# Kernel tuning notes

Measured on AMD Instinct MI355X. Metric: run time of the kernel, lower is better.

Reference implementation:

```python
import jax, jax.numpy as jnp
import numpy as np

# hyperparams (from init_kwargs / opt)
POS_W, NEG_W = 2.0, 40.0
MARGIN, THRESH = 0.1, 0.5
TAU, ALPHA, BETA = 4.0, 1.0, 0.5
N_EPOCHS = 100
F_STANDARD = False
N_CLASSES = 100


def setup_inputs() -> dict:
    key = jax.random.key(0)
    k1, k2, k3 = jax.random.split(key, 3)
    B, D = 4096, 128
    batch = jax.random.normal(k1, (B, D), dtype=jnp.float32)
    batch = batch / jnp.linalg.norm(batch, axis=1, keepdims=True)
    teacher = jax.random.normal(k2, (B, D), dtype=jnp.float32)
    teacher = teacher / jnp.linalg.norm(teacher, axis=1, keepdims=True)
    labels = jax.random.randint(k3, (B,), 0, N_CLASSES, dtype=jnp.int64 if jax.config.jax_enable_x64 else jnp.int32)
    return {"batch": batch, "teacher_batch": teacher, "labels": labels, "epoch": 50}


def reference(batch, teacher_batch, labels, epoch):
    B = batch.shape[0]
    sim = batch @ batch.T                              # [B,B]
    same = labels[:, None] == labels[None, :]          # [B,B]
    eye = jnp.eye(B, dtype=bool)
    pos = same & ~eye
    neg = ~same

    inf = jnp.float32(jnp.inf)
    min_pos = jnp.min(jnp.where(pos, sim, inf), axis=1)    # [B]
    max_neg = jnp.max(jnp.where(neg, sim, -inf), axis=1)   # [B]
    neg_keep = neg & (sim + MARGIN > min_pos[:, None])
    pos_keep = pos & (sim - MARGIN < max_neg[:, None])
    valid = jnp.any(neg_keep, axis=1) & jnp.any(pos_keep, axis=1)

    # masked log-sum-exp terms; exp(-inf)=0 keeps masked entries (and grads) zero
    pos_term = (1.0 / POS_W) * jnp.log1p(
        jnp.sum(jnp.exp(jnp.where(pos_keep, -POS_W * (sim - THRESH), -inf)), axis=1))
    neg_term = (1.0 / NEG_W) * jnp.log1p(
        jnp.sum(jnp.exp(jnp.where(neg_keep, NEG_W * (sim - THRESH), -inf)), axis=1))
    n_valid = jnp.maximum(jnp.sum(valid.astype(sim.dtype)), 1.0)
    loss_rank = jnp.sum(jnp.where(valid, pos_term + neg_term, 0.0)) / n_valid

    # KD term: per-anchor concat(pos_sims, neg_sims) is a permutation of the full
    # row, and softmax/KL are permutation invariant -> apply per-element scaling.
    t_sim = teacher_batch @ teacher_batch.T
    scale = jnp.ones_like(sim) if F_STANDARD else jnp.where(neg, BETA, 1.0)
    log_p = jax.nn.log_softmax(sim * scale / TAU, axis=1)
    q = jax.lax.stop_gradient(jax.nn.softmax(t_sim * scale / TAU, axis=1))
    # KLDivLoss(batchmean) on a [1,B] row == sum(q * (log q - log_p))
    kl_rows = jnp.sum(q * (jnp.log(q) - log_p), axis=1)   # [B]
    loss_kd = jnp.mean(kl_rows)

    loss = loss_rank + (epoch / N_EPOCHS) * ALPHA * (TAU ** 2) * loss_kd
    return (loss, loss_rank, loss_kd)
```

## Files before the change

kernel.cpp:

```cpp
#include <hip/hip_runtime.h>
#include <hip/hip_fp16.h>
#include <math.h>

#define BB  4096
#define DD  128
#define NCH 16
#define NP  8
#define TB  256

typedef __attribute__((ext_vector_type(8))) _Float16 half8;
typedef __attribute__((ext_vector_type(4))) float f32x4;

constexpr float POS_W  = 2.0f;
constexpr float NEG_W  = 40.0f;
constexpr float MARGIN = 0.1f;
constexpr float THRESH = 0.5f;

__device__ __forceinline__ unsigned short f2h(float f) {
  __half h = __float2half(f);
  return __half_as_ushort(h);
}
__device__ __forceinline__ f32x4 mfma16h(half8 a, half8 b, f32x4 c) {
  return __builtin_amdgcn_mfma_f32_16x16x32_f16(a, b, c, 0, 0, 0);
}
__device__ __forceinline__ void gll16(const void* g, void* l) {
  __builtin_amdgcn_global_load_lds(
      (const __attribute__((address_space(1))) void*)g,
      (__attribute__((address_space(3))) void*)l, 16, 0, 0);
}

__global__ __launch_bounds__(256) void k0(
    const float* __restrict__ b, const float* __restrict__ t,
    unsigned short* __restrict__ xf, unsigned short* __restrict__ yf)
{
  const int i = blockIdx.x * 256 + threadIdx.x;
  {
    float4 v = reinterpret_cast<const float4*>(b)[i];
    ushort4 h;
    h.x = f2h(v.x); h.y = f2h(v.y); h.z = f2h(v.z); h.w = f2h(v.w);
    reinterpret_cast<ushort4*>(xf)[i] = h;
  }
  {
    float4 v = reinterpret_cast<const float4*>(t)[i];
    ushort4 h;
    h.x = f2h(v.x); h.y = f2h(v.y); h.z = f2h(v.z); h.w = f2h(v.w);
    reinterpret_cast<ushort4*>(yf)[i] = h;
  }
}


__global__ __launch_bounds__(TB, 3) void kA(
    const unsigned short* __restrict__ xf,
    const int* __restrict__ labels,
    float* __restrict__ mpP, float* __restrict__ mnP, float* __restrict__ zsP)
{
  __shared__ unsigned short sX[2][4096];
  __shared__ int sJlab[256];

  const int tid  = threadIdx.x;
  const int lane = tid & 63;
  const int wid  = tid >> 6;
  const int ag   = blockIdx.x & 31;
  const int ch   = blockIdx.x >> 5;
  const int i0w  = ag * 128 + wid * 32;
  const int l15  = lane & 15;
  const int hi_l = lane >> 4;
  const int rbase = hi_l * 4;
  const int koff  = hi_l * 8;
  const int j0ch  = ch * 256;
  const int srow  = lane & 31;
  const int sk0   = wid * 32 + (lane >> 5) * 8;

  sJlab[tid] = labels[j0ch + tid];

  half8 Ax[2][4];
#pragma unroll
  for (int at = 0; at < 2; ++at) {
    const size_t ab = (size_t)(i0w + at * 16 + l15) * DD + koff;
#pragma unroll
    for (int s = 0; s < 4; ++s)
      Ax[at][s] = *reinterpret_cast<const half8*>(xf + ab + s * 32);
  }
  int labA[2][4];
#pragma unroll
  for (int at = 0; at < 2; ++at)
#pragma unroll
    for (int r = 0; r < 4; ++r) labA[at][r] = labels[i0w + at * 16 + rbase + r];

  float mp[2][4], mn[2][4], zs[2][4];
#pragma unroll
  for (int at = 0; at < 2; ++at)
#pragma unroll
    for (int r = 0; r < 4; ++r) { mp[at][r] = INFINITY; mn[at][r] = -INFINITY; zs[at][r] = 0.f; }

  {
    const size_t g0 = (size_t)(j0ch + srow) * DD + sk0;
    gll16(xf + g0,      &sX[0][wid * 1024]);
    gll16(xf + g0 + 16, &sX[0][wid * 1024 + 512]);
  }

#pragma unroll 1
  for (int pp = 0; pp < NP; ++pp) {
    const int cur = pp & 1;
    __syncthreads();
    if (pp + 1 < NP) {
      const size_t g0 = (size_t)(j0ch + (pp + 1) * 32 + srow) * DD + sk0;
      gll16(xf + g0,      &sX[cur ^ 1][wid * 1024]);
      gll16(xf + g0 + 16, &sX[cur ^ 1][wid * 1024 + 512]);
    }

    f32x4 acc[2][2];
#pragma unroll
    for (int at = 0; at < 2; ++at)
#pragma unroll
      for (int t = 0; t < 2; ++t) acc[at][t] = {0.f, 0.f, 0.f, 0.f};
#pragma unroll
    for (int s = 0; s < 4; ++s) {
#pragma unroll
      for (int t = 0; t < 2; ++t) {
        const int ro = (s * 128 + hi_l * 32 + t * 16 + l15) * 8;
        half8 vB = *reinterpret_cast<const half8*>(&sX[cur][ro]);
        acc[0][t] = mfma16h(Ax[0][s], vB, acc[0][t]);
        acc[1][t] = mfma16h(Ax[1][s], vB, acc[1][t]);
      }
    }

#pragma unroll
    for (int t = 0; t < 2; ++t) {
      const int lj   = sJlab[pp * 32 + t * 16 + l15];
      const int jcol = j0ch + pp * 32 + t * 16 + l15;
#pragma unroll
      for (int at = 0; at < 2; ++at)
#pragma unroll
        for (int r = 0; r < 4; ++r) {
          float sim = acc[at][t][r];
          bool same = (lj == labA[at][r]);
          zs[at][r] += __expf(sim * (same ? 0.25f : 0.125f));
          if (same) {
            if (jcol != i0w + at * 16 + rbase + r) mp[at][r] = fminf(mp[at][r], sim);
          } else {
            mn[at][r] = fmaxf(mn[at][r], sim);
          }
        }
    }
  }

#pragma unroll
  for (int at = 0; at < 2; ++at)
#pragma unroll
    for (int r = 0; r < 4; ++r)
#pragma unroll
      for (int m = 1; m < 16; m <<= 1) {
        mp[at][r] = fminf(mp[at][r], __shfl_xor(mp[at][r], m));
        mn[at][r] = fmaxf(mn[at][r], __shfl_xor(mn[at][r], m));
        zs[at][r] += __shfl_xor(zs[at][r], m);
      }
  if (l15 == 0) {
#pragma unroll
    for (int at = 0; at < 2; ++at)
#pragma unroll
      for (int r = 0; r < 4; ++r) {
        const int i_r = i0w + at * 16 + rbase + r;
        mpP[ch * BB + i_r] = mp[at][r];
        mnP[ch * BB + i_r] = mn[at][r];
        zsP[ch * BB + i_r] = zs[at][r];
      }
  }
}

__global__ __launch_bounds__(256) void kR(
    const float* __restrict__ mpP, const float* __restrict__ mnP,
    const float* __restrict__ zsP,
    float* __restrict__ mpg, float* __restrict__ mng, float* __restrict__ zsg,
    int* __restrict__ cnt)
{
  const int i = blockIdx.x * 256 + threadIdx.x;
  if (i == 0) *cnt = 0;
  float a = INFINITY, b = -INFINITY, c = 0.f;
#pragma unroll
  for (int ch = 0; ch < NCH; ++ch) {
    a = fminf(a, mpP[ch * BB + i]);
    b = fmaxf(b, mnP[ch * BB + i]);
    c += zsP[ch * BB + i];
  }
  mpg[i] = a; mng[i] = b; zsg[i] = c;
}

__global__ __launch_bounds__(TB, 2) void kB(
    const unsigned short* __restrict__ xf, const unsigned short* __restrict__ yf,
    const int* __restrict__ labels,
    const float* __restrict__ mpg, const float* __restrict__ mng,
    float* __restrict__ ztP, float* __restrict__ wvP,
    float* __restrict__ psP, float* __restrict__ nsP)
{
  __shared__ unsigned short sB[2][8192];
  __shared__ int sJlab[256];

  const int tid  = threadIdx.x;
  const int lane = tid & 63;
  const int wid  = tid >> 6;
  const int ag   = blockIdx.x & 31;
  const int ch   = blockIdx.x >> 5;
  const int i0w  = ag * 128 + wid * 32;
  const int l15  = lane & 15;
  const int hi_l = lane >> 4;
  const int rbase = hi_l * 4;
  const int koff  = hi_l * 8;
  const int j0ch  = ch * 256;
  const int srow  = lane & 31;
  const int sk0   = wid * 32 + (lane >> 5) * 8;

  sJlab[tid] = labels[j0ch + tid];

  half8 Ax[2][4], Ay[2][4];
#pragma unroll
  for (int at = 0; at < 2; ++at) {
    const size_t ab = (size_t)(i0w + at * 16 + l15) * DD + koff;
#pragma unroll
    for (int s = 0; s < 4; ++s) {
      Ax[at][s] = *reinterpret_cast<const half8*>(xf + ab + s * 32);
      Ay[at][s] = *reinterpret_cast<const half8*>(yf + ab + s * 32);
    }
  }
  int labA[2][4]; float mpA[2][4], mnA[2][4];
#pragma unroll
  for (int at = 0; at < 2; ++at)
#pragma unroll
    for (int r = 0; r < 4; ++r) {
      const int i_r = i0w + at * 16 + rbase + r;
      labA[at][r] = labels[i_r];
      mpA[at][r]  = mpg[i_r];
      mnA[at][r]  = mng[i_r];
    }

  float zt[2][4], wv[2][4], ps[2][4], ns[2][4];
#pragma unroll
  for (int at = 0; at < 2; ++at)
#pragma unroll
    for (int r = 0; r < 4; ++r) { zt[at][r] = 0.f; wv[at][r] = 0.f; ps[at][r] = 0.f; ns[at][r] = 0.f; }

  {
    const size_t g0 = (size_t)(j0ch + srow) * DD + sk0;
    gll16(xf + g0,      &sB[0][wid * 1024]);
    gll16(xf + g0 + 16, &sB[0][wid * 1024 + 512]);
    gll16(yf + g0,      &sB[0][4096 + wid * 1024]);
    gll16(yf + g0 + 16, &sB[0][4096 + wid * 1024 + 512]);
  }

#pragma unroll 1
  for (int pp = 0; pp < NP; ++pp) {
    const int cur = pp & 1;
    __syncthreads();
    if (pp + 1 < NP) {
      const size_t g0 = (size_t)(j0ch + (pp + 1) * 32 + srow) * DD + sk0;
      gll16(xf + g0,      &sB[cur ^ 1][wid * 1024]);
      gll16(xf + g0 + 16, &sB[cur ^ 1][wid * 1024 + 512]);
      gll16(yf + g0,      &sB[cur ^ 1][4096 + wid * 1024]);
      gll16(yf + g0 + 16, &sB[cur ^ 1][4096 + wid * 1024 + 512]);
    }

    f32x4 aS[2][2], aT[2][2];
#pragma unroll
    for (int at = 0; at < 2; ++at)
#pragma unroll
      for (int t = 0; t < 2; ++t) { aS[at][t] = {0.f,0.f,0.f,0.f}; aT[at][t] = {0.f,0.f,0.f,0.f}; }
#pragma unroll
    for (int s = 0; s < 4; ++s) {
#pragma unroll
      for (int t = 0; t < 2; ++t) {
        const int ro = (s * 128 + hi_l * 32 + t * 16 + l15) * 8;
        half8 vX = *reinterpret_cast<const half8*>(&sB[cur][ro]);
        half8 vY = *reinterpret_cast<const half8*>(&sB[cur][4096 + ro]);
        aS[0][t] = mfma16h(Ax[0][s], vX, aS[0][t]);
        aS[1][t] = mfma16h(Ax[1][s], vX, aS[1][t]);
        aT[0][t] = mfma16h(Ay[0][s], vY, aT[0][t]);
        aT[1][t] = mfma16h(Ay[1][s], vY, aT[1][t]);
      }
    }

#pragma unroll
    for (int t = 0; t < 2; ++t) {
      const int lj   = sJlab[pp * 32 + t * 16 + l15];
      const int jcol = j0ch + pp * 32 + t * 16 + l15;
#pragma unroll
      for (int at = 0; at < 2; ++at)
#pragma unroll
        for (int r = 0; r < 4; ++r) {
          float sim = aS[at][t][r], ts0 = aT[at][t][r];
          bool same = (lj == labA[at][r]);
          float sc = same ? 0.25f : 0.125f;
          float s  = sim * sc;
          float ts = ts0 * sc;
          float et = __expf(ts);
          zt[at][r] += et;
          wv[at][r] += et * (ts - s);
          if (same) {
            if (jcol != i0w + at * 16 + rbase + r && (sim - MARGIN < mnA[at][r]))
              ps[at][r] += __expf(-POS_W * (sim - THRESH));
          } else {
            if (sim + MARGIN > mpA[at][r])
              ns[at][r] += __expf(NEG_W * (sim - THRESH));
          }
        }
    }
  }

#pragma unroll
  for (int at = 0; at < 2; ++at)
#pragma unroll
    for (int r = 0; r < 4; ++r)
#pragma unroll
      for (int m = 1; m < 16; m <<= 1) {
        zt[at][r] += __shfl_xor(zt[at][r], m);
        wv[at][r] += __shfl_xor(wv[at][r], m);
        ps[at][r] += __shfl_xor(ps[at][r], m);
        ns[at][r] += __shfl_xor(ns[at][r], m);
      }
  if (l15 == 0) {
#pragma unroll
    for (int at = 0; at < 2; ++at)
#pragma unroll
      for (int r = 0; r < 4; ++r) {
        const int i_r = i0w + at * 16 + rbase + r;
        ztP[ch * BB + i_r] = zt[at][r];
        wvP[ch * BB + i_r] = wv[at][r];
        psP[ch * BB + i_r] = ps[at][r];
        nsP[ch * BB + i_r] = ns[at][r];
      }
  }
}

__global__ __launch_bounds__(512) void kD(
    const float* __restrict__ zsg, const float* __restrict__ ztP,
    const float* __restrict__ wvP, const float* __restrict__ psP,
    const float* __restrict__ nsP, const int* __restrict__ epoch,
    double* __restrict__ rkP, double* __restrict__ kdP, int* __restrict__ nvP,
    int* __restrict__ cnt, float* __restrict__ out)
{
  __shared__ double sR[8], sK[8];
  __shared__ int    sN[8];
  const int tid = threadIdx.x;
  const int lane = tid & 63;
  const int wid = tid >> 6;
  const int i = blockIdx.x * 512 + tid;

  float zt = 0.f, wv = 0.f, ps = 0.f, ns = 0.f;
#pragma unroll
  for (int c = 0; c < NCH; ++c) {
    zt += ztP[c * BB + i];
    wv += wvP[c * BB + i];
    ps += psP[c * BB + i];
    ns += nsP[c * BB + i];
  }
  float zs = zsg[i];
  double kd = (double)(wv / zt + __logf(zs) - __logf(zt));
  double rank = 0.0; int nv = 0;
  if (ps > 0.f && ns > 0.f) {
    rank = (double)(log1pf(ps) * 0.5f + log1pf(ns) * 0.025f);
    nv = 1;
  }
#pragma unroll
  for (int o = 32; o; o >>= 1) {
    rank += __shfl_xor(rank, o);
    kd   += __shfl_xor(kd, o);
    nv   += __shfl_xor(nv, o);
  }
  if (lane == 0) { sR[wid] = rank; sK[wid] = kd; sN[wid] = nv; }
  __syncthreads();
  if (tid == 0) {
    double R_ = 0.0, K_ = 0.0; int N_ = 0;
    for (int w = 0; w < 8; ++w) { R_ += sR[w]; K_ += sK[w]; N_ += sN[w]; }
    rkP[blockIdx.x] = R_;
    kdP[blockIdx.x] = K_;
    nvP[blockIdx.x] = N_;
    __threadfence();
    int old = atomicAdd(cnt, 1);
    if (old == 7) {
      __threadfence();
      double RT = 0.0, KT = 0.0; int NT = 0;
      for (int b = 0; b < 8; ++b) { RT += rkP[b]; KT += kdP[b]; NT += nvP[b]; }
      double loss_rank = RT / (double)(NT < 1 ? 1 : NT);
      double loss_kd   = KT / (double)BB;
      double wgt = (double)epoch[0] * 0.16;
      out[0] = (float)(loss_rank + wgt * loss_kd);
      out[1] = (float)loss_rank;
      out[2] = (float)loss_kd;
      *cnt = 0;
    }
  }
}

extern "C" void kernel_launch(void* const* d_in, const int* in_sizes, int n_in,
                              void* d_out, int out_size, void* d_ws, size_t ws_size,
                              hipStream_t stream)
{
  (void)in_sizes; (void)n_in; (void)out_size; (void)ws_size;
  const float* batch   = (const float*)d_in[0];
  const float* teacher = (const float*)d_in[1];
  const int*   labels  = (const int*)d_in[2];
  const int*   epoch   = (const int*)d_in[3];
  float* out = (float*)d_out;

  char* w = (char*)d_ws;
  const size_t MB = 1048576;
  unsigned short* xf = (unsigned short*)(w + 0 * MB);
  unsigned short* yf = (unsigned short*)(w + 1 * MB);
  const size_t PCH = (size_t)NCH * BB * sizeof(float);
  float* mpP = (float*)(w + 2 * MB + 0 * PCH);
  float* mnP = (float*)(w + 2 * MB + 1 * PCH);
  float* zsP = (float*)(w + 2 * MB + 2 * PCH);
  float* ztP = (float*)(w + 2 * MB + 3 * PCH);
  float* wvP = (float*)(w + 2 * MB + 4 * PCH);
  float* psP = (float*)(w + 2 * MB + 5 * PCH);
  float* nsP = (float*)(w + 2 * MB + 6 * PCH);
  float* mpg = (float*)(w + 4 * MB);
  float* mng = (float*)(w + 4 * MB + 16384);
  float* zsg = (float*)(w + 4 * MB + 32768);
  double* rkP = (double*)(w + 4 * MB + 49152);
  double* kdP = (double*)(w + 4 * MB + 49152 + 64);
  int*    nvP = (int*)(w + 4 * MB + 49152 + 128);
  int*    cnt = (int*)(w + 4 * MB + 49152 + 192);

  k0<<<dim3(BB * DD / 4 / 256), dim3(256), 0, stream>>>(batch, teacher, xf, yf);
  kA<<<dim3(32 * NCH), dim3(TB), 0, stream>>>(xf, labels, mpP, mnP, zsP);
  kR<<<dim3(BB / 256), dim3(256), 0, stream>>>(mpP, mnP, zsP, mpg, mng, zsg, cnt);
  kB<<<dim3(32 * NCH), dim3(TB), 0, stream>>>(xf, yf, labels, mpg, mng,
                                              ztP, wvP, psP, nsP);
  kD<<<dim3(8), dim3(512), 0, stream>>>(zsg, ztP, wvP, psP, nsP, epoch,
                                        rkP, kdP, nvP, cnt, out);
}
```

Before: 63.48 us.

## Move teacher GEMM into first pass and fold min/max reduction into second pass

The teacher similarity GEMM and its softmax partial sums move from the second similarity pass into the first, which now computes student and teacher tiles together. The separate reduction kernel kR is removed: the second pass reduces the per-chunk min-positive and max-negative partials itself into shared memory, and kD sums the zs partials directly. The counter reset moves into the conversion kernel. This saves one launch and rebalances work between the passes, but the first pass now carries more registers and LDS at lower occupancy, and every block of the second pass repeats the chunk reduction for its 128 anchors.

```diff
diff --git a/kernel.cpp b/kernel.cpp
--- a/kernel.cpp
+++ b/kernel.cpp
@@ -31,9 +31,11 @@
 
 __global__ __launch_bounds__(256) void k0(
     const float* __restrict__ b, const float* __restrict__ t,
-    unsigned short* __restrict__ xf, unsigned short* __restrict__ yf)
+    unsigned short* __restrict__ xf, unsigned short* __restrict__ yf,
+    int* __restrict__ cnt)
 {
   const int i = blockIdx.x * 256 + threadIdx.x;
+  if (i == 0) *cnt = 0;
   {
     float4 v = reinterpret_cast<const float4*>(b)[i];
     ushort4 h;
@@ -49,12 +51,13 @@
 }
 
 
-__global__ __launch_bounds__(TB, 3) void kA(
-    const unsigned short* __restrict__ xf,
+__global__ __launch_bounds__(TB, 2) void kG1(
+    const unsigned short* __restrict__ xf, const unsigned short* __restrict__ yf,
     const int* __restrict__ labels,
-    float* __restrict__ mpP, float* __restrict__ mnP, float* __restrict__ zsP)
+    float* __restrict__ zsP, float* __restrict__ mpP, float* __restrict__ mnP,
+    float* __restrict__ ztP, float* __restrict__ wvP)
 {
-  __shared__ unsigned short sX[2][4096];
+  __shared__ unsigned short sB[2][8192];
   __shared__ int sJlab[256];
 
   const int tid  = threadIdx.x;
@@ -73,13 +76,15 @@
 
   sJlab[tid] = labels[j0ch + tid];
 
-  half8 Ax[2][4];
+  half8 Ax[2][4], Ay[2][4];
 #pragma unroll
   for (int at = 0; at < 2; ++at) {
     const size_t ab = (size_t)(i0w + at * 16 + l15) * DD + koff;
 #pragma unroll
-    for (int s = 0; s < 4; ++s)
+    for (int s = 0; s < 4; ++s) {
       Ax[at][s] = *reinterpret_cast<const half8*>(xf + ab + s * 32);
+      Ay[at][s] = *reinterpret_cast<const half8*>(yf + ab + s * 32);
+    }
   }
   int labA[2][4];
 #pragma unroll
@@ -87,16 +92,21 @@
 #pragma unroll
     for (int r = 0; r < 4; ++r) labA[at][r] = labels[i0w + at * 16 + rbase + r];
 
-  float mp[2][4], mn[2][4], zs[2][4];
-#pragma unroll
-  for (int at = 0; at < 2; ++at)
-#pragma unroll
-    for (int r = 0; r < 4; ++r) { mp[at][r] = INFINITY; mn[at][r] = -INFINITY; zs[at][r] = 0.f; }
+  float zs[2][4], mp[2][4], mn[2][4], zt[2][4], wv[2][4];
+#pragma unroll
+  for (int at = 0; at < 2; ++at)
+#pragma unroll
+    for (int r = 0; r < 4; ++r) {
+      zs[at][r] = 0.f; mp[at][r] = INFINITY; mn[at][r] = -INFINITY;
+      zt[at][r] = 0.f; wv[at][r] = 0.f;
+    }
 
   {
     const size_t g0 = (size_t)(j0ch + srow) * DD + sk0;
-    gll16(xf + g0,      &sX[0][wid * 1024]);
-    gll16(xf + g0 + 16, &sX[0][wid * 1024 + 512]);
+    gll16(xf + g0,      &sB[0][wid * 1024]);
+    gll16(xf + g0 + 16, &sB[0][wid * 1024 + 512]);
+    gll16(yf + g0,      &sB[0][4096 + wid * 1024]);
+    gll16(yf + g0 + 16, &sB[0][4096 + wid * 1024 + 512]);
   }
 
 #pragma unroll 1
@@ -105,23 +115,28 @@
     __syncthreads();
     if (pp + 1 < NP) {
       const size_t g0 = (size_t)(j0ch + (pp + 1) * 32 + srow) * DD + sk0;
-      gll16(xf + g0,      &sX[cur ^ 1][wid * 1024]);
-      gll16(xf + g0 + 16, &sX[cur ^ 1][wid * 1024 + 512]);
-    }
-
-    f32x4 acc[2][2];
+      gll16(xf + g0,      &sB[cur ^ 1][wid * 1024]);
+      gll16(xf + g0 + 16, &sB[cur ^ 1][wid * 1024 + 512]);
+      gll16(yf + g0,      &sB[cur ^ 1][4096 + wid * 1024]);
+      gll16(yf + g0 + 16, &sB[cur ^ 1][4096 + wid * 1024 + 512]);
+    }
+
+    f32x4 aS[2][2], aT[2][2];
 #pragma unroll
     for (int at = 0; at < 2; ++at)
 #pragma unroll
-      for (int t = 0; t < 2; ++t) acc[at][t] = {0.f, 0.f, 0.f, 0.f};
+      for (int t = 0; t < 2; ++t) { aS[at][t] = {0.f,0.f,0.f,0.f}; aT[at][t] = {0.f,0.f,0.f,0.f}; }
 #pragma unroll
     for (int s = 0; s < 4; ++s) {
 #pragma unroll
       for (int t = 0; t < 2; ++t) {
         const int ro = (s * 128 + hi_l * 32 + t * 16 + l15) * 8;
-        half8 vB = *reinterpret_cast<const half8*>(&sX[cur][ro]);
-        acc[0][t] = mfma16h(Ax[0][s], vB, acc[0][t]);
-        acc[1][t] = mfma16h(Ax[1][s], vB, acc[1][t]);
+        half8 vX = *reinterpret_cast<const half8*>(&sB[cur][ro]);
+        half8 vY = *reinterpret_cast<const half8*>(&sB[cur][4096 + ro]);
+        aS[0][t] = mfma16h(Ax[0][s], vX, aS[0][t]);
+        aS[1][t] = mfma16h(Ax[1][s], vX, aS[1][t]);
+        aT[0][t] = mfma16h(Ay[0][s], vY, aT[0][t]);
+        aT[1][t] = mfma16h(Ay[1][s], vY, aT[1][t]);
       }
     }
 
@@ -133,9 +148,15 @@
       for (int at = 0; at < 2; ++at)
 #pragma unroll
         for (int r = 0; r < 4; ++r) {
-          float sim = acc[at][t][r];
+          float sim = aS[at][t][r], tsim = aT[at][t][r];
           bool same = (lj == labA[at][r]);
-          zs[at][r] += __expf(sim * (same ? 0.25f : 0.125f));
+          float sc = same ? 0.25f : 0.125f;
+          float s  = sim * sc;
+          float ts = tsim * sc;
+          zs[at][r] += __expf(s);
+          float et = __expf(ts);
+          zt[at][r] += et;
+          wv[at][r] += et * (ts - s);
           if (same) {
             if (jcol != i0w + at * 16 + rbase + r) mp[at][r] = fminf(mp[at][r], sim);
           } else {
@@ -151,9 +172,11 @@
     for (int r = 0; r < 4; ++r)
 #pragma unroll
       for (int m = 1; m < 16; m <<= 1) {
+        zs[at][r] += __shfl_xor(zs[at][r], m);
         mp[at][r] = fminf(mp[at][r], __shfl_xor(mp[at][r], m));
         mn[at][r] = fmaxf(mn[at][r], __shfl_xor(mn[at][r], m));
-        zs[at][r] += __shfl_xor(zs[at][r], m);
+        zt[at][r] += __shfl_xor(zt[at][r], m);
+        wv[at][r] += __shfl_xor(wv[at][r], m);
       }
   if (l15 == 0) {
 #pragma unroll
@@ -161,40 +184,24 @@
 #pragma unroll
       for (int r = 0; r < 4; ++r) {
         const int i_r = i0w + at * 16 + rbase + r;
+        zsP[ch * BB + i_r] = zs[at][r];
         mpP[ch * BB + i_r] = mp[at][r];
         mnP[ch * BB + i_r] = mn[at][r];
-        zsP[ch * BB + i_r] = zs[at][r];
-      }
-  }
-}
-
-__global__ __launch_bounds__(256) void kR(
+        ztP[ch * BB + i_r] = zt[at][r];
+        wvP[ch * BB + i_r] = wv[at][r];
+      }
+  }
+}
+
+__global__ __launch_bounds__(TB, 3) void kG2(
+    const unsigned short* __restrict__ xf,
+    const int* __restrict__ labels,
     const float* __restrict__ mpP, const float* __restrict__ mnP,
-    const float* __restrict__ zsP,
-    float* __restrict__ mpg, float* __restrict__ mng, float* __restrict__ zsg,
-    int* __restrict__ cnt)
-{
-  const int i = blockIdx.x * 256 + threadIdx.x;
-  if (i == 0) *cnt = 0;
-  float a = INFINITY, b = -INFINITY, c = 0.f;
-#pragma unroll
-  for (int ch = 0; ch < NCH; ++ch) {
-    a = fminf(a, mpP[ch * BB + i]);
-    b = fmaxf(b, mnP[ch * BB + i]);
-    c += zsP[ch * BB + i];
-  }
-  mpg[i] = a; mng[i] = b; zsg[i] = c;
-}
-
-__global__ __launch_bounds__(TB, 2) void kB(
-    const unsigned short* __restrict__ xf, const unsigned short* __restrict__ yf,
-    const int* __restrict__ labels,
-    const float* __restrict__ mpg, const float* __restrict__ mng,
-    float* __restrict__ ztP, float* __restrict__ wvP,
     float* __restrict__ psP, float* __restrict__ nsP)
 {
-  __shared__ unsigned short sB[2][8192];
+  __shared__ unsigned short sX[2][4096];
   __shared__ int sJlab[256];
+  __shared__ float sMPr[128], sMNr[128];
 
   const int tid  = threadIdx.x;
   const int lane = tid & 63;
@@ -210,42 +217,54 @@
   const int srow  = lane & 31;
   const int sk0   = wid * 32 + (lane >> 5) * 8;
 
+  {
+    const size_t g0 = (size_t)(j0ch + srow) * DD + sk0;
+    gll16(xf + g0,      &sX[0][wid * 1024]);
+    gll16(xf + g0 + 16, &sX[0][wid * 1024 + 512]);
+  }
+
   sJlab[tid] = labels[j0ch + tid];
-
-  half8 Ax[2][4], Ay[2][4];
+  if (tid < 128) {
+    const int aidx = ag * 128 + tid;
+    float a = INFINITY, b = -INFINITY;
+#pragma unroll
+    for (int c = 0; c < NCH; ++c) {
+      a = fminf(a, mpP[c * BB + aidx]);
+      b = fmaxf(b, mnP[c * BB + aidx]);
+    }
+    sMPr[tid] = a; sMNr[tid] = b;
+  }
+
+  half8 Ax[2][4];
 #pragma unroll
   for (int at = 0; at < 2; ++at) {
     const size_t ab = (size_t)(i0w + at * 16 + l15) * DD + koff;
 #pragma unroll
-    for (int s = 0; s < 4; ++s) {
+    for (int s = 0; s < 4; ++s)
       Ax[at][s] = *reinterpret_cast<const half8*>(xf + ab + s * 32);
-      Ay[at][s] = *reinterpret_cast<const half8*>(yf + ab + s * 32);
-    }
-  }
-  int labA[2][4]; float mpA[2][4], mnA[2][4];
+  }
+  int labA[2][4];
+#pragma unroll
+  for (int at = 0; at < 2; ++at)
+#pragma unroll
+    for (int r = 0; r < 4; ++r) labA[at][r] = labels[i0w + at * 16 + rbase + r];
+
+  __syncthreads();
+  float mpA[2][4], mnA[2][4];
 #pragma unroll
   for (int at = 0; at < 2; ++at)
 #pragma unroll
     for (int r = 0; r < 4; ++r) {
-      const int i_r = i0w + at * 16 + rbase + r;
-      labA[at][r] = labels[i_r];
-      mpA[at][r]  = mpg[i_r];
-      mnA[at][r]  = mng[i_r];
-    }
-
-  float zt[2][4], wv[2][4], ps[2][4], ns[2][4];
-#pragma unroll
-  for (int at = 0; at < 2; ++at)
-#pragma unroll
-    for (int r = 0; r < 4; ++r) { zt[at][r] = 0.f; wv[at][r] = 0.f; ps[at][r] = 0.f; ns[at][r] = 0.f; }
-
-  {
-    const size_t g0 = (size_t)(j0ch + srow) * DD + sk0;
-    gll16(xf + g0,      &sB[0][wid * 1024]);
-    gll16(xf + g0 + 16, &sB[0][wid * 1024 + 512]);
-    gll16(yf + g0,      &sB[0][4096 + wid * 1024]);
-    gll16(yf + g0 + 16, &sB[0][4096 + wid * 1024 + 512]);
-  }
+      const int al = wid * 32 + at * 16 + rbase + r;
+      mpA[at][r] = sMPr[al];
+      mnA[at][r] = sMNr[al];
+    }
+
+  float ps[2][4], ns[2][4];
+#pragma unroll
+  for (int at = 0; at < 2; ++at)
+#pragma unroll
+    for (int r = 0; r < 4; ++r) { ps[at][r] = 0.f; ns[at][r] = 0.f; }
 
 #pragma unroll 1
   for (int pp = 0; pp < NP; ++pp) {
@@ -253,28 +272,23 @@
     __syncthreads();
     if (pp + 1 < NP) {
       const size_t g0 = (size_t)(j0ch + (pp + 1) * 32 + srow) * DD + sk0;
-      gll16(xf + g0,      &sB[cur ^ 1][wid * 1024]);
-      gll16(xf + g0 + 16, &sB[cur ^ 1][wid * 1024 + 512]);
-      gll16(yf + g0,      &sB[cur ^ 1][4096 + wid * 1024]);
-      gll16(yf + g0 + 16, &sB[cur ^ 1][4096 + wid * 1024 + 512]);
-    }
-
-    f32x4 aS[2][2], aT[2][2];
+      gll16(xf + g0,      &sX[cur ^ 1][wid * 1024]);
+      gll16(xf + g0 + 16, &sX[cur ^ 1][wid * 1024 + 512]);
+    }
+
+    f32x4 acc[2][2];
 #pragma unroll
     for (int at = 0; at < 2; ++at)
 #pragma unroll
-      for (int t = 0; t < 2; ++t) { aS[at][t] = {0.f,0.f,0.f,0.f}; aT[at][t] = {0.f,0.f,0.f,0.f}; }
+      for (int t = 0; t < 2; ++t) acc[at][t] = {0.f, 0.f, 0.f, 0.f};
 #pragma unroll
     for (int s = 0; s < 4; ++s) {
 #pragma unroll
       for (int t = 0; t < 2; ++t) {
         const int ro = (s * 128 + hi_l * 32 + t * 16 + l15) * 8;
-        half8 vX = *reinterpret_cast<const half8*>(&sB[cur][ro]);
-        half8 vY = *reinterpret_cast<const half8*>(&sB[cur][4096 + ro]);
-        aS[0][t] = mfma16h(Ax[0][s], vX, aS[0][t]);
-        aS[1][t] = mfma16h(Ax[1][s], vX, aS[1][t]);
-        aT[0][t] = mfma16h(Ay[0][s], vY, aT[0][t]);
-        aT[1][t] = mfma16h(Ay[1][s], vY, aT[1][t]);
+        half8 vB = *reinterpret_cast<const half8*>(&sX[cur][ro]);
+        acc[0][t] = mfma16h(Ax[0][s], vB, acc[0][t]);
+        acc[1][t] = mfma16h(Ax[1][s], vB, acc[1][t]);
       }
     }
 
@@ -286,14 +300,8 @@
       for (int at = 0; at < 2; ++at)
 #pragma unroll
         for (int r = 0; r < 4; ++r) {
-          float sim = aS[at][t][r], ts0 = aT[at][t][r];
+          float sim = acc[at][t][r];
           bool same = (lj == labA[at][r]);
-          float sc = same ? 0.25f : 0.125f;
-          float s  = sim * sc;
-          float ts = ts0 * sc;
-          float et = __expf(ts);
-          zt[at][r] += et;
-          wv[at][r] += et * (ts - s);
           if (same) {
             if (jcol != i0w + at * 16 + rbase + r && (sim - MARGIN < mnA[at][r]))
               ps[at][r] += __expf(-POS_W * (sim - THRESH));
@@ -311,8 +319,6 @@
     for (int r = 0; r < 4; ++r)
 #pragma unroll
       for (int m = 1; m < 16; m <<= 1) {
-        zt[at][r] += __shfl_xor(zt[at][r], m);
-        wv[at][r] += __shfl_xor(wv[at][r], m);
         ps[at][r] += __shfl_xor(ps[at][r], m);
         ns[at][r] += __shfl_xor(ns[at][r], m);
       }
@@ -322,8 +328,6 @@
 #pragma unroll
       for (int r = 0; r < 4; ++r) {
         const int i_r = i0w + at * 16 + rbase + r;
-        ztP[ch * BB + i_r] = zt[at][r];
-        wvP[ch * BB + i_r] = wv[at][r];
         psP[ch * BB + i_r] = ps[at][r];
         nsP[ch * BB + i_r] = ns[at][r];
       }
@@ -331,7 +335,7 @@
 }
 
 __global__ __launch_bounds__(512) void kD(
-    const float* __restrict__ zsg, const float* __restrict__ ztP,
+    const float* __restrict__ zsP, const float* __restrict__ ztP,
     const float* __restrict__ wvP, const float* __restrict__ psP,
     const float* __restrict__ nsP, const int* __restrict__ epoch,
     double* __restrict__ rkP, double* __restrict__ kdP, int* __restrict__ nvP,
@@ -344,15 +348,15 @@
   const int wid = tid >> 6;
   const int i = blockIdx.x * 512 + tid;
 
-  float zt = 0.f, wv = 0.f, ps = 0.f, ns = 0.f;
+  float zs = 0.f, zt = 0.f, wv = 0.f, ps = 0.f, ns = 0.f;
 #pragma unroll
   for (int c = 0; c < NCH; ++c) {
+    zs += zsP[c * BB + i];
     zt += ztP[c * BB + i];
     wv += wvP[c * BB + i];
     ps += psP[c * BB + i];
     ns += nsP[c * BB + i];
   }
-  float zs = zsg[i];
   double kd = (double)(wv / zt + __logf(zs) - __logf(zt));
   double rank = 0.0; int nv = 0;
   if (ps > 0.f && ns > 0.f) {
@@ -406,26 +410,22 @@
   unsigned short* xf = (unsigned short*)(w + 0 * MB);
   unsigned short* yf = (unsigned short*)(w + 1 * MB);
   const size_t PCH = (size_t)NCH * BB * sizeof(float);
-  float* mpP = (float*)(w + 2 * MB + 0 * PCH);
-  float* mnP = (float*)(w + 2 * MB + 1 * PCH);
-  float* zsP = (float*)(w + 2 * MB + 2 * PCH);
+  float* zsP = (float*)(w + 2 * MB + 0 * PCH);
+  float* mpP = (float*)(w + 2 * MB + 1 * PCH);
+  float* mnP = (float*)(w + 2 * MB + 2 * PCH);
   float* ztP = (float*)(w + 2 * MB + 3 * PCH);
   float* wvP = (float*)(w + 2 * MB + 4 * PCH);
   float* psP = (float*)(w + 2 * MB + 5 * PCH);
   float* nsP = (float*)(w + 2 * MB + 6 * PCH);
-  float* mpg = (float*)(w + 4 * MB);
-  float* mng = (float*)(w + 4 * MB + 16384);
-  float* zsg = (float*)(w + 4 * MB + 32768);
-  double* rkP = (double*)(w + 4 * MB + 49152);
-  double* kdP = (double*)(w + 4 * MB + 49152 + 64);
-  int*    nvP = (int*)(w + 4 * MB + 49152 + 128);
-  int*    cnt = (int*)(w + 4 * MB + 49152 + 192);
-
-  k0<<<dim3(BB * DD / 4 / 256), dim3(256), 0, stream>>>(batch, teacher, xf, yf);
-  kA<<<dim3(32 * NCH), dim3(TB), 0, stream>>>(xf, labels, mpP, mnP, zsP);
-  kR<<<dim3(BB / 256), dim3(256), 0, stream>>>(mpP, mnP, zsP, mpg, mng, zsg, cnt);
-  kB<<<dim3(32 * NCH), dim3(TB), 0, stream>>>(xf, yf, labels, mpg, mng,
-                                              ztP, wvP, psP, nsP);
-  kD<<<dim3(8), dim3(512), 0, stream>>>(zsg, ztP, wvP, psP, nsP, epoch,
+  double* rkP = (double*)(w + 4 * MB);
+  double* kdP = (double*)(w + 4 * MB + 64);
+  int*    nvP = (int*)(w + 4 * MB + 128);
+  int*    cnt = (int*)(w + 4 * MB + 192);
+
+  k0<<<dim3(BB * DD / 4 / 256), dim3(256), 0, stream>>>(batch, teacher, xf, yf, cnt);
+  kG1<<<dim3(32 * NCH), dim3(TB), 0, stream>>>(xf, yf, labels,
+                                               zsP, mpP, mnP, ztP, wvP);
+  kG2<<<dim3(32 * NCH), dim3(TB), 0, stream>>>(xf, labels, mpP, mnP, psP, nsP);
+  kD<<<dim3(8), dim3(512), 0, stream>>>(zsP, ztP, wvP, psP, nsP, epoch,
                                         rkP, kdP, nvP, cnt, out);
 }
```

Result: faster. 59.30 us (-6.6%).
